# Performance work log

Hardware: AMD Instinct MI355X
Metric: run time of the kernel (lower is better)

The kernel has to match this reference:

```python
import jax, jax.numpy as jnp
import numpy as np
from jax import lax

N, H, BS = 256, 1024, 128
ALPHA, BETA, SIGMA = 60.0, 20.0, 5.0
EPS = 1e-8


def _mlp_w(key, n_in, n_out):
    return jax.random.normal(key, (n_out, n_in), dtype=jnp.float32) / np.sqrt(n_in)


def setup_inputs() -> dict:
    key = jax.random.key(0)
    ks = jax.random.split(key, 8)
    inp = {
        "t": jnp.zeros((), dtype=jnp.float32),
        "x": jax.random.normal(ks[0], (BS, N), dtype=jnp.float32),
        "Wf1": _mlp_w(ks[1], N, H), "bf1": jnp.zeros((H,), jnp.float32),
        "Wf2": _mlp_w(ks[2], H, N), "bf2": jnp.zeros((N,), jnp.float32),
        "Wg1": _mlp_w(ks[3], N, H), "bg1": jnp.zeros((H,), jnp.float32),
        "Wg2": _mlp_w(ks[4], H, N), "bg2": jnp.zeros((N,), jnp.float32),
        "Wk1": _mlp_w(ks[5], N, H), "bk1": jnp.zeros((H,), jnp.float32),
        "Wk2": _mlp_w(ks[6], H, N), "bk2": jnp.zeros((N,), jnp.float32),
    }
    return inp


def reference(t, x, Wf1, bf1, Wf2, bf2, Wg1, bg1, Wg2, bg2, Wk1, bk1, Wk2, bk2):
    def mlp(u, W1, b1, W2, b2):
        return jnp.tanh(u @ W1.T + b1) @ W2.T + b2

    def k_func(u):
        return mlp(u, Wk1, bk1, Wk2, bk2)

    f_out = mlp(x, Wf1, bf1, Wf2, bf2)          # f_model(t, x); t unused
    k_out = k_func(x)
    G_k_out = mlp(x, Wg1, bg1, Wg2, bg2)        # g_fn(x)[0]
    dx_dt = f_out + G_k_out

    # compute_k_jacobian: torch detaches u, so no grad flows to x here.
    # torch layout: J[b, j, i] = d k_i / d u_j  (transpose of jacfwd output)
    x_d = lax.stop_gradient(x)
    J_fwd = jax.vmap(jax.jacfwd(k_func))(x_d)   # [bs, i_out, j_in]
    J_x = jnp.swapaxes(J_fwd, 1, 2)             # [bs, j, i]

    k_norm = jnp.linalg.norm(k_out, axis=1)                      # [bs]
    Jf = jnp.einsum('bji,bi->bj', J_x, f_out)                    # bmm(J, f)
    Jf_norm = jnp.linalg.norm(Jf, axis=1)
    c1 = Jf_norm - ALPHA * k_norm ** (2 * SIGMA - 1)
    JG = jnp.einsum('bji,bi->bj', J_x, G_k_out)                  # bmm(J, G)
    c2 = jnp.sum(k_out * JG, axis=1) - BETA * k_norm ** (2 * SIGMA)

    mask = (c1 > EPS) | (c2 < -EPS)                              # [bs]
    dx_upd = jnp.where(mask[:, None], jnp.zeros_like(dx_dt), dx_dt)
    return (dx_upd + dx_dt) / 2
```

## Files before the change

kernel.cpp:

```cpp
#include <hip/hip_runtime.h>
#include <stdint.h>

#define N_ 256
#define H_ 1024
#define BS_ 128

#define WS_T    0
#define WS_SK   393216
#define WS_OACC 524288
#define WS_SFV  622592
#define WS_SGV  753664
#define WS_JACC 884736
#define WS_FLOATS 950272

__global__ __launch_bounds__(256) void k1_layer1(
    const float* __restrict__ x,
    const float* __restrict__ Wf1, const float* __restrict__ bf1,
    const float* __restrict__ Wg1, const float* __restrict__ bg1,
    const float* __restrict__ Wk1, const float* __restrict__ bk1,
    float* __restrict__ T, float* __restrict__ sk)
{
    const int bx = blockIdx.x;
    const int m  = bx >> 7;
    const int ht = (bx & 127) >> 5;
    const int rt = bx & 31;
    const int t  = threadIdx.x;
    const int r0 = rt * 4;
    const int h  = ht * 256 + t;

    const float* W  = (m == 0) ? Wf1 : (m == 1) ? Wg1 : Wk1;
    const float* b1 = (m == 0) ? bf1 : (m == 1) ? bg1 : bk1;

    __shared__ float xs[4][256];
    #pragma unroll
    for (int rr = 0; rr < 4; ++rr)
        xs[rr][t] = x[(r0 + rr) * N_ + t];
    __syncthreads();

    float acc[4];
    const float bv = b1[h];
    acc[0] = acc[1] = acc[2] = acc[3] = bv;
    const float4* w4 = (const float4*)(W + h * N_);
    #pragma unroll 4
    for (int c = 0; c < 64; ++c) {
        float4 w = w4[c];
        #pragma unroll
        for (int rr = 0; rr < 4; ++rr) {
            float4 a = ((const float4*)xs[rr])[c];
            acc[rr] += w.x * a.x + w.y * a.y + w.z * a.z + w.w * a.w;
        }
    }
    float* Tm = T + (m * BS_ + r0) * H_;
    #pragma unroll
    for (int rr = 0; rr < 4; ++rr) {
        float v = tanhf(acc[rr]);
        Tm[rr * H_ + h] = v;
        if (m == 2) sk[(r0 + rr) * H_ + h] = 1.0f - v * v;
    }
}

__global__ __launch_bounds__(256) void k2_layer2(
    const float* __restrict__ T,
    const float* __restrict__ Wf2, const float* __restrict__ bf2,
    const float* __restrict__ Wg2, const float* __restrict__ bg2,
    const float* __restrict__ Wk2, const float* __restrict__ bk2,
    float* __restrict__ oacc)
{
    const int bx = blockIdx.x;
    const int m  = bx >> 7;
    const int rt = (bx & 127) >> 2;
    const int ks = bx & 3;
    const int t  = threadIdx.x;
    const int r0 = rt * 4;
    const int h0 = ks * 256;

    const float* W  = (m == 0) ? Wf2 : (m == 1) ? Wg2 : Wk2;
    const float* b2 = (m == 0) ? bf2 : (m == 1) ? bg2 : bk2;

    __shared__ float ts[4][256];
    #pragma unroll
    for (int rr = 0; rr < 4; ++rr)
        ts[rr][t] = T[(m * BS_ + r0 + rr) * H_ + h0 + t];
    __syncthreads();

    float acc[4];
    const float bv = (ks == 0) ? b2[t] : 0.0f;
    acc[0] = acc[1] = acc[2] = acc[3] = bv;
    const float4* w4 = (const float4*)(W + t * H_ + h0);
    #pragma unroll 4
    for (int c = 0; c < 64; ++c) {
        float4 w = w4[c];
        #pragma unroll
        for (int rr = 0; rr < 4; ++rr) {
            float4 a = ((const float4*)ts[rr])[c];
            acc[rr] += w.x * a.x + w.y * a.y + w.z * a.z + w.w * a.w;
        }
    }
    #pragma unroll
    for (int rr = 0; rr < 4; ++rr)
        atomicAdd(&oacc[(m * BS_ + r0 + rr) * N_ + t], acc[rr]);
}

__global__ __launch_bounds__(256) void k3_v(
    const float* __restrict__ Wk2,
    const float* __restrict__ oacc,
    const float* __restrict__ sk,
    float* __restrict__ sfv, float* __restrict__ sgv)
{
    const int bx = blockIdx.x;
    const int r  = bx >> 2;
    const int ht = bx & 3;
    const int t  = threadIdx.x;
    const int h  = ht * 256 + t;

    __shared__ float fos[256], gos[256];
    fos[t] = oacc[r * N_ + t];
    gos[t] = oacc[(BS_ + r) * N_ + t];
    __syncthreads();

    float af = 0.f, ag = 0.f;
    const float* w = Wk2 + h;
    #pragma unroll 8
    for (int i = 0; i < 256; ++i) {
        float wv = w[i * H_];
        af += wv * fos[i];
        ag += wv * gos[i];
    }
    const float s = sk[r * H_ + h];
    sfv[r * H_ + h] = s * af;
    sgv[r * H_ + h] = s * ag;
}

__global__ __launch_bounds__(256) void k4_j(
    const float* __restrict__ Wk1,
    const float* __restrict__ sfv, const float* __restrict__ sgv,
    float* __restrict__ jacc)
{
    const int bx = blockIdx.x;
    const int r  = bx >> 2;
    const int ks = bx & 3;
    const int t  = threadIdx.x;
    const int h0 = ks * 256;

    __shared__ float sf[256], sg[256];
    sf[t] = sfv[r * H_ + h0 + t];
    sg[t] = sgv[r * H_ + h0 + t];
    __syncthreads();

    float aJf = 0.f, aJg = 0.f;
    const float* w = Wk1 + h0 * N_ + t;
    #pragma unroll 8
    for (int hh = 0; hh < 256; ++hh) {
        float wv = w[hh * N_];
        aJf += sf[hh] * wv;
        aJg += sg[hh] * wv;
    }
    atomicAdd(&jacc[r * N_ + t], aJf);
    atomicAdd(&jacc[(BS_ + r) * N_ + t], aJg);
}

__global__ __launch_bounds__(256) void k5_final(
    const float* __restrict__ oacc,
    const float* __restrict__ jacc,
    float* __restrict__ out)
{
    const int r = blockIdx.x;
    const int t = threadIdx.x;
    __shared__ float red[12];

    const float fo = oacc[r * N_ + t];
    const float go = oacc[(BS_ + r) * N_ + t];
    const float ko = oacc[(2 * BS_ + r) * N_ + t];
    const float jf = jacc[r * N_ + t];
    const float jg = jacc[(BS_ + r) * N_ + t];

    float v0 = ko * ko;
    float v1 = jf * jf;
    float v2 = ko * jg;
    #pragma unroll
    for (int o = 32; o > 0; o >>= 1) {
        v0 += __shfl_xor(v0, o, 64);
        v1 += __shfl_xor(v1, o, 64);
        v2 += __shfl_xor(v2, o, 64);
    }
    const int wid = t >> 6;
    if ((t & 63) == 0) {
        red[wid * 3 + 0] = v0;
        red[wid * 3 + 1] = v1;
        red[wid * 3 + 2] = v2;
    }
    __syncthreads();
    const float kn2 = red[0] + red[3] + red[6] + red[9];
    const float jf2 = red[1] + red[4] + red[7] + red[10];
    const float kjg = red[2] + red[5] + red[8] + red[11];

    const float knorm = sqrtf(kn2);
    const float kn4 = kn2 * kn2;
    const float kn8 = kn4 * kn4;
    const float c1 = sqrtf(jf2) - 60.0f * kn8 * knorm;
    const float c2 = kjg - 20.0f * kn8 * kn2;
    const bool mask = (c1 > 1e-8f) || (c2 < -1e-8f);
    const float scale = mask ? 0.5f : 1.0f;

    out[r * N_ + t] = (fo + go) * scale;
}

__global__ __launch_bounds__(256) void manifold_fused(
    const float* __restrict__ x,
    const float* __restrict__ Wf1, const float* __restrict__ bf1v,
    const float* __restrict__ Wf2, const float* __restrict__ bf2v,
    const float* __restrict__ Wg1, const float* __restrict__ bg1v,
    const float* __restrict__ Wg2, const float* __restrict__ bg2v,
    const float* __restrict__ Wk1, const float* __restrict__ bk1v,
    const float* __restrict__ Wk2, const float* __restrict__ bk2v,
    float* __restrict__ out)
{
    const int b = blockIdx.x;
    const int t = threadIdx.x;
    __shared__ float xs[N_];
    __shared__ float tf[H_], tg[H_], tk[H_], sk[H_];
    __shared__ float fo[N_], go[N_];
    __shared__ float sfv[H_], sgv[H_];
    __shared__ float red[12];

    xs[t] = x[b * N_ + t];
    __syncthreads();
    {
        float acc[12];
        const float4* rows[12];
        #pragma unroll
        for (int m = 0; m < 4; ++m) {
            const int h = t + m * 256;
            rows[m]     = (const float4*)(Wf1 + h * N_);
            rows[4 + m] = (const float4*)(Wg1 + h * N_);
            rows[8 + m] = (const float4*)(Wk1 + h * N_);
            acc[m] = bf1v[h]; acc[4 + m] = bg1v[h]; acc[8 + m] = bk1v[h];
        }
        const float4* xs4 = (const float4*)xs;
        #pragma unroll 2
        for (int c = 0; c < 64; ++c) {
            float4 a = xs4[c];
            #pragma unroll
            for (int r = 0; r < 12; ++r) {
                float4 w = rows[r][c];
                acc[r] += w.x * a.x + w.y * a.y + w.z * a.z + w.w * a.w;
            }
        }
        #pragma unroll
        for (int m = 0; m < 4; ++m) {
            const int h = t + m * 256;
            float vtf = tanhf(acc[m]);
            float vtg = tanhf(acc[4 + m]);
            float vtk = tanhf(acc[8 + m]);
            tf[h] = vtf; tg[h] = vtg; tk[h] = vtk; sk[h] = 1.0f - vtk * vtk;
        }
    }
    __syncthreads();
    float af = bf2v[t], ag = bg2v[t], ak = bk2v[t];
    {
        const float4* rf = (const float4*)(Wf2 + t * H_);
        const float4* rg = (const float4*)(Wg2 + t * H_);
        const float4* rk = (const float4*)(Wk2 + t * H_);
        #pragma unroll 2
        for (int c = 0; c < 256; ++c) {
            float4 wf = rf[c], wg = rg[c], wk = rk[c];
            float4 vf = ((const float4*)tf)[c];
            af += wf.x*vf.x + wf.y*vf.y + wf.z*vf.z + wf.w*vf.w;
            float4 vg = ((const float4*)tg)[c];
            ag += wg.x*vg.x + wg.y*vg.y + wg.z*vg.z + wg.w*vg.w;
            float4 vk = ((const float4*)tk)[c];
            ak += wk.x*vk.x + wk.y*vk.y + wk.z*vk.z + wk.w*vk.w;
        }
    }
    fo[t] = af; go[t] = ag;
    __syncthreads();
    {
        float vf[4] = {0.f,0.f,0.f,0.f}, vg[4] = {0.f,0.f,0.f,0.f};
        const float* base = Wk2 + 4 * t;
        #pragma unroll 4
        for (int i = 0; i < N_; ++i) {
            float4 w = *(const float4*)(base + i * H_);
            float fv = fo[i], gv = go[i];
            vf[0]+=w.x*fv; vf[1]+=w.y*fv; vf[2]+=w.z*fv; vf[3]+=w.w*fv;
            vg[0]+=w.x*gv; vg[1]+=w.y*gv; vg[2]+=w.z*gv; vg[3]+=w.w*gv;
        }
        #pragma unroll
        for (int c = 0; c < 4; ++c) {
            sfv[4*t+c] = sk[4*t+c]*vf[c];
            sgv[4*t+c] = sk[4*t+c]*vg[c];
        }
    }
    __syncthreads();
    float jf = 0.f, jg = 0.f;
    {
        const float* col = Wk1 + t;
        #pragma unroll 4
        for (int c = 0; c < 256; ++c) {
            float4 s4 = ((const float4*)sfv)[c];
            float4 g4 = ((const float4*)sgv)[c];
            const int h = c * 4;
            float w0 = col[(h+0)*N_], w1 = col[(h+1)*N_];
            float w2 = col[(h+2)*N_], w3 = col[(h+3)*N_];
            jf += s4.x*w0 + s4.y*w1 + s4.z*w2 + s4.w*w3;
            jg += g4.x*w0 + g4.y*w1 + g4.z*w2 + g4.w*w3;
        }
    }
    float v0 = ak*ak, v1 = jf*jf, v2 = ak*jg;
    #pragma unroll
    for (int o = 32; o > 0; o >>= 1) {
        v0 += __shfl_xor(v0, o, 64);
        v1 += __shfl_xor(v1, o, 64);
        v2 += __shfl_xor(v2, o, 64);
    }
    const int wid = t >> 6;
    if ((t & 63) == 0) {
        red[wid*3+0] = v0; red[wid*3+1] = v1; red[wid*3+2] = v2;
    }
    __syncthreads();
    const float kn2 = red[0]+red[3]+red[6]+red[9];
    const float jf2 = red[1]+red[4]+red[7]+red[10];
    const float kjg = red[2]+red[5]+red[8]+red[11];
    const float knorm = sqrtf(kn2);
    const float kn4 = kn2*kn2, kn8 = kn4*kn4;
    const float c1 = sqrtf(jf2) - 60.0f*kn8*knorm;
    const float c2 = kjg - 20.0f*kn8*kn2;
    const float scale = ((c1 > 1e-8f) || (c2 < -1e-8f)) ? 0.5f : 1.0f;
    out[b*N_+t] = (af+ag)*scale;
}

extern "C" void kernel_launch(void* const* d_in, const int* in_sizes, int n_in,
                              void* d_out, int out_size, void* d_ws, size_t ws_size,
                              hipStream_t stream) {
    const float* x    = (const float*)d_in[1];
    const float* Wf1  = (const float*)d_in[2];
    const float* bf1v = (const float*)d_in[3];
    const float* Wf2  = (const float*)d_in[4];
    const float* bf2v = (const float*)d_in[5];
    const float* Wg1  = (const float*)d_in[6];
    const float* bg1v = (const float*)d_in[7];
    const float* Wg2  = (const float*)d_in[8];
    const float* bg2v = (const float*)d_in[9];
    const float* Wk1  = (const float*)d_in[10];
    const float* bk1v = (const float*)d_in[11];
    const float* Wk2  = (const float*)d_in[12];
    const float* bk2v = (const float*)d_in[13];
    float* out = (float*)d_out;

    if (ws_size < (size_t)WS_FLOATS * sizeof(float)) {
        manifold_fused<<<BS_, 256, 0, stream>>>(
            x, Wf1, bf1v, Wf2, bf2v, Wg1, bg1v, Wg2, bg2v,
            Wk1, bk1v, Wk2, bk2v, out);
        return;
    }

    float* ws   = (float*)d_ws;
    float* T    = ws + WS_T;
    float* sk   = ws + WS_SK;
    float* oacc = ws + WS_OACC;
    float* sfv  = ws + WS_SFV;
    float* sgv  = ws + WS_SGV;
    float* jacc = ws + WS_JACC;

    hipMemsetAsync(oacc, 0, 3 * BS_ * N_ * sizeof(float), stream);
    hipMemsetAsync(jacc, 0, 2 * BS_ * N_ * sizeof(float), stream);

    k1_layer1<<<384, 256, 0, stream>>>(x, Wf1, bf1v, Wg1, bg1v, Wk1, bk1v, T, sk);
    k2_layer2<<<384, 256, 0, stream>>>(T, Wf2, bf2v, Wg2, bg2v, Wk2, bk2v, oacc);
    k3_v     <<<512, 256, 0, stream>>>(Wk2, oacc, sk, sfv, sgv);
    k4_j     <<<512, 256, 0, stream>>>(Wk1, sfv, sgv, jacc);
    k5_final <<<BS_, 256, 0, stream>>>(oacc, jacc, out);
}
```

Measured before the change: 143.1 us.

## Double grid sizes, fold memsets into kernels, restructure Wk2 product with coalesced atomics

Halves the rows per block in both layer kernels so twice as many blocks run, and zeroes the accumulation buffers inside the first two kernels instead of issuing separate memsets. The Wk2-transpose product is rewritten to read Wk2 rows as coalesced float4 and split the reduction over 8 slices with atomic accumulation. The tanh-derivative scaling moves into the Jacobian kernel, which now uses 128-row slices. This aims for better occupancy, coalesced loads and fewer launches. In exchange it adds more atomics and re-reads the weights more often.

```diff
diff --git a/kernel.cpp b/kernel.cpp
--- a/kernel.cpp
+++ b/kernel.cpp
@@ -8,8 +8,7 @@
 #define WS_T    0
 #define WS_SK   393216
 #define WS_OACC 524288
-#define WS_SFV  622592
-#define WS_SGV  753664
+#define WS_VACC 622592
 #define WS_JACC 884736
 #define WS_FLOATS 950272
 
@@ -18,44 +17,45 @@
     const float* __restrict__ Wf1, const float* __restrict__ bf1,
     const float* __restrict__ Wg1, const float* __restrict__ bg1,
     const float* __restrict__ Wk1, const float* __restrict__ bk1,
-    float* __restrict__ T, float* __restrict__ sk)
+    float* __restrict__ T, float* __restrict__ sk,
+    float* __restrict__ oacc, float* __restrict__ vacc)
 {
     const int bx = blockIdx.x;
-    const int m  = bx >> 7;
-    const int ht = (bx & 127) >> 5;
-    const int rt = bx & 31;
+    const int m  = bx >> 8;
+    const int ht = (bx & 255) >> 6;
+    const int rp = bx & 63;
     const int t  = threadIdx.x;
-    const int r0 = rt * 4;
+    const int r0 = rp * 2;
     const int h  = ht * 256 + t;
+
+    const int gtid = bx * 256 + t;
+    if (gtid < 3 * BS_ * N_) oacc[gtid] = 0.0f;
+    for (int idx = gtid; idx < 2 * BS_ * H_; idx += 768 * 256) vacc[idx] = 0.0f;
 
     const float* W  = (m == 0) ? Wf1 : (m == 1) ? Wg1 : Wk1;
     const float* b1 = (m == 0) ? bf1 : (m == 1) ? bg1 : bk1;
 
-    __shared__ float xs[4][256];
-    #pragma unroll
-    for (int rr = 0; rr < 4; ++rr)
-        xs[rr][t] = x[(r0 + rr) * N_ + t];
-    __syncthreads();
-
-    float acc[4];
-    const float bv = b1[h];
-    acc[0] = acc[1] = acc[2] = acc[3] = bv;
+    __shared__ float xs[2][256];
+    xs[0][t] = x[r0 * N_ + t];
+    xs[1][t] = x[(r0 + 1) * N_ + t];
+    __syncthreads();
+
+    float a0 = b1[h], a1 = a0;
     const float4* w4 = (const float4*)(W + h * N_);
-    #pragma unroll 4
+    #pragma unroll 8
     for (int c = 0; c < 64; ++c) {
-        float4 w = w4[c];
-        #pragma unroll
-        for (int rr = 0; rr < 4; ++rr) {
-            float4 a = ((const float4*)xs[rr])[c];
-            acc[rr] += w.x * a.x + w.y * a.y + w.z * a.z + w.w * a.w;
-        }
-    }
-    float* Tm = T + (m * BS_ + r0) * H_;
-    #pragma unroll
-    for (int rr = 0; rr < 4; ++rr) {
-        float v = tanhf(acc[rr]);
-        Tm[rr * H_ + h] = v;
-        if (m == 2) sk[(r0 + rr) * H_ + h] = 1.0f - v * v;
+        float4 w  = w4[c];
+        float4 xa = ((const float4*)xs[0])[c];
+        float4 xb = ((const float4*)xs[1])[c];
+        a0 += w.x * xa.x + w.y * xa.y + w.z * xa.z + w.w * xa.w;
+        a1 += w.x * xb.x + w.y * xb.y + w.z * xb.z + w.w * xb.w;
+    }
+    const float v0 = tanhf(a0), v1 = tanhf(a1);
+    T[(m * BS_ + r0) * H_ + h]     = v0;
+    T[(m * BS_ + r0 + 1) * H_ + h] = v1;
+    if (m == 2) {
+        sk[r0 * H_ + h]       = 1.0f - v0 * v0;
+        sk[(r0 + 1) * H_ + h] = 1.0f - v1 * v1;
     }
 }
 
@@ -64,94 +64,97 @@
     const float* __restrict__ Wf2, const float* __restrict__ bf2,
     const float* __restrict__ Wg2, const float* __restrict__ bg2,
     const float* __restrict__ Wk2, const float* __restrict__ bk2,
-    float* __restrict__ oacc)
+    float* __restrict__ oacc, float* __restrict__ jacc)
 {
     const int bx = blockIdx.x;
-    const int m  = bx >> 7;
-    const int rt = (bx & 127) >> 2;
+    const int m  = bx >> 8;
+    const int rp = (bx & 255) >> 2;
     const int ks = bx & 3;
     const int t  = threadIdx.x;
-    const int r0 = rt * 4;
+    const int r0 = rp * 2;
     const int h0 = ks * 256;
+
+    const int gtid = bx * 256 + t;
+    if (gtid < 2 * BS_ * N_) jacc[gtid] = 0.0f;
 
     const float* W  = (m == 0) ? Wf2 : (m == 1) ? Wg2 : Wk2;
     const float* b2 = (m == 0) ? bf2 : (m == 1) ? bg2 : bk2;
 
-    __shared__ float ts[4][256];
-    #pragma unroll
-    for (int rr = 0; rr < 4; ++rr)
-        ts[rr][t] = T[(m * BS_ + r0 + rr) * H_ + h0 + t];
-    __syncthreads();
-
-    float acc[4];
+    __shared__ float ts[2][256];
+    ts[0][t] = T[(m * BS_ + r0) * H_ + h0 + t];
+    ts[1][t] = T[(m * BS_ + r0 + 1) * H_ + h0 + t];
+    __syncthreads();
+
     const float bv = (ks == 0) ? b2[t] : 0.0f;
-    acc[0] = acc[1] = acc[2] = acc[3] = bv;
+    float a0 = bv, a1 = bv;
     const float4* w4 = (const float4*)(W + t * H_ + h0);
-    #pragma unroll 4
+    #pragma unroll 8
     for (int c = 0; c < 64; ++c) {
-        float4 w = w4[c];
-        #pragma unroll
-        for (int rr = 0; rr < 4; ++rr) {
-            float4 a = ((const float4*)ts[rr])[c];
-            acc[rr] += w.x * a.x + w.y * a.y + w.z * a.z + w.w * a.w;
-        }
-    }
-    #pragma unroll
-    for (int rr = 0; rr < 4; ++rr)
-        atomicAdd(&oacc[(m * BS_ + r0 + rr) * N_ + t], acc[rr]);
+        float4 w  = w4[c];
+        float4 ta = ((const float4*)ts[0])[c];
+        float4 tb = ((const float4*)ts[1])[c];
+        a0 += w.x * ta.x + w.y * ta.y + w.z * ta.z + w.w * ta.w;
+        a1 += w.x * tb.x + w.y * tb.y + w.z * tb.z + w.w * tb.w;
+    }
+    atomicAdd(&oacc[(m * BS_ + r0) * N_ + t], a0);
+    atomicAdd(&oacc[(m * BS_ + r0 + 1) * N_ + t], a1);
 }
 
 __global__ __launch_bounds__(256) void k3_v(
     const float* __restrict__ Wk2,
     const float* __restrict__ oacc,
-    const float* __restrict__ sk,
-    float* __restrict__ sfv, float* __restrict__ sgv)
-{
-    const int bx = blockIdx.x;
-    const int r  = bx >> 2;
-    const int ht = bx & 3;
-    const int t  = threadIdx.x;
-    const int h  = ht * 256 + t;
-
-    __shared__ float fos[256], gos[256];
-    fos[t] = oacc[r * N_ + t];
-    gos[t] = oacc[(BS_ + r) * N_ + t];
-    __syncthreads();
-
-    float af = 0.f, ag = 0.f;
-    const float* w = Wk2 + h;
+    float* __restrict__ vacc)
+{
+    const int r   = blockIdx.x >> 3;
+    const int isl = blockIdx.x & 7;
+    const int t   = threadIdx.x;
+    const int i0  = isl * 32;
+
+    __shared__ float fos[32], gos[32];
+    if (t < 32)       fos[t]      = oacc[r * N_ + i0 + t];
+    else if (t < 64)  gos[t - 32] = oacc[(BS_ + r) * N_ + i0 + (t - 32)];
+    __syncthreads();
+
+    float4 af = {0.f, 0.f, 0.f, 0.f};
+    float4 ag = {0.f, 0.f, 0.f, 0.f};
     #pragma unroll 8
-    for (int i = 0; i < 256; ++i) {
-        float wv = w[i * H_];
-        af += wv * fos[i];
-        ag += wv * gos[i];
-    }
-    const float s = sk[r * H_ + h];
-    sfv[r * H_ + h] = s * af;
-    sgv[r * H_ + h] = s * ag;
+    for (int ii = 0; ii < 32; ++ii) {
+        float4 w = ((const float4*)(Wk2 + (i0 + ii) * H_))[t];
+        const float fv = fos[ii], gv = gos[ii];
+        af.x += w.x * fv; af.y += w.y * fv; af.z += w.z * fv; af.w += w.w * fv;
+        ag.x += w.x * gv; ag.y += w.y * gv; ag.z += w.z * gv; ag.w += w.w * gv;
+    }
+    float* vf = vacc + r * H_ + 4 * t;
+    atomicAdd(vf + 0, af.x); atomicAdd(vf + 1, af.y);
+    atomicAdd(vf + 2, af.z); atomicAdd(vf + 3, af.w);
+    float* vg = vacc + (BS_ + r) * H_ + 4 * t;
+    atomicAdd(vg + 0, ag.x); atomicAdd(vg + 1, ag.y);
+    atomicAdd(vg + 2, ag.z); atomicAdd(vg + 3, ag.w);
 }
 
 __global__ __launch_bounds__(256) void k4_j(
     const float* __restrict__ Wk1,
-    const float* __restrict__ sfv, const float* __restrict__ sgv,
+    const float* __restrict__ vacc, const float* __restrict__ sk,
     float* __restrict__ jacc)
 {
-    const int bx = blockIdx.x;
-    const int r  = bx >> 2;
-    const int ks = bx & 3;
+    const int r  = blockIdx.x >> 3;
+    const int ks = blockIdx.x & 7;
     const int t  = threadIdx.x;
-    const int h0 = ks * 256;
-
-    __shared__ float sf[256], sg[256];
-    sf[t] = sfv[r * H_ + h0 + t];
-    sg[t] = sgv[r * H_ + h0 + t];
+    const int h0 = ks * 128;
+
+    __shared__ float sf[128], sg[128];
+    if (t < 128) sf[t] = sk[r * H_ + h0 + t] * vacc[r * H_ + h0 + t];
+    else {
+        const int u = t - 128;
+        sg[u] = sk[r * H_ + h0 + u] * vacc[(BS_ + r) * H_ + h0 + u];
+    }
     __syncthreads();
 
     float aJf = 0.f, aJg = 0.f;
     const float* w = Wk1 + h0 * N_ + t;
     #pragma unroll 8
-    for (int hh = 0; hh < 256; ++hh) {
-        float wv = w[hh * N_];
+    for (int hh = 0; hh < 128; ++hh) {
+        const float wv = w[hh * N_];
         aJf += sf[hh] * wv;
         aJg += sg[hh] * wv;
     }
@@ -199,8 +202,7 @@
     const float kn8 = kn4 * kn4;
     const float c1 = sqrtf(jf2) - 60.0f * kn8 * knorm;
     const float c2 = kjg - 20.0f * kn8 * kn2;
-    const bool mask = (c1 > 1e-8f) || (c2 < -1e-8f);
-    const float scale = mask ? 0.5f : 1.0f;
+    const float scale = ((c1 > 1e-8f) || (c2 < -1e-8f)) ? 0.5f : 1.0f;
 
     out[r * N_ + t] = (fo + go) * scale;
 }
@@ -357,16 +359,14 @@
     float* T    = ws + WS_T;
     float* sk   = ws + WS_SK;
     float* oacc = ws + WS_OACC;
-    float* sfv  = ws + WS_SFV;
-    float* sgv  = ws + WS_SGV;
+    float* vacc = ws + WS_VACC;
     float* jacc = ws + WS_JACC;
 
-    hipMemsetAsync(oacc, 0, 3 * BS_ * N_ * sizeof(float), stream);
-    hipMemsetAsync(jacc, 0, 2 * BS_ * N_ * sizeof(float), stream);
-
-    k1_layer1<<<384, 256, 0, stream>>>(x, Wf1, bf1v, Wg1, bg1v, Wk1, bk1v, T, sk);
-    k2_layer2<<<384, 256, 0, stream>>>(T, Wf2, bf2v, Wg2, bg2v, Wk2, bk2v, oacc);
-    k3_v     <<<512, 256, 0, stream>>>(Wk2, oacc, sk, sfv, sgv);
-    k4_j     <<<512, 256, 0, stream>>>(Wk1, sfv, sgv, jacc);
+    k1_layer1<<<768, 256, 0, stream>>>(x, Wf1, bf1v, Wg1, bg1v, Wk1, bk1v,
+                                       T, sk, oacc, vacc);
+    k2_layer2<<<768, 256, 0, stream>>>(T, Wf2, bf2v, Wg2, bg2v, Wk2, bk2v,
+                                       oacc, jacc);
+    k3_v     <<<1024, 256, 0, stream>>>(Wk2, oacc, vacc);
+    k4_j     <<<1024, 256, 0, stream>>>(Wk1, vacc, sk, jacc);
     k5_final <<<BS_, 256, 0, stream>>>(oacc, jacc, out);
 }
```

Result: slower. 176.6 us (+23.5%).
